# Kernel tuning notes

Hardware: AMD Instinct MI355X
Metric: run time of the kernel (lower is better)

## Reference

```python
import jax, jax.numpy as jnp
import numpy as np
import math

B, T = 8, 1024
IN_DIMS = 1024
OUT_DIMS = 1024
NUM_CODES = 1024
NUM_CODEBOOKS = 8


def setup_inputs() -> dict:
    key = jax.random.key(0)
    k1, k2, k3, k4, k5 = jax.random.split(key, 5)
    x = jax.random.normal(k1, (B, T, IN_DIMS), dtype=jnp.float32)
    target = jax.random.randint(k2, (B, T, NUM_CODEBOOKS), 0, NUM_CODES, dtype=jnp.int64)
    # params, init per reset_params()
    codebook = jax.random.normal(k3, (NUM_CODES, NUM_CODEBOOKS, OUT_DIMS), dtype=jnp.float32) / math.sqrt(OUT_DIMS * NUM_CODEBOOKS)
    proj_w = jax.random.normal(k4, (NUM_CODEBOOKS * NUM_CODES, IN_DIMS), dtype=jnp.float32) / math.sqrt(IN_DIMS)
    proj_b = jnp.zeros((NUM_CODEBOOKS * NUM_CODES,), dtype=jnp.float32)
    wproj_w = jax.random.normal(k5, (NUM_CODEBOOKS, IN_DIMS), dtype=jnp.float32) / math.sqrt(IN_DIMS)
    return {"x": x, "target": target, "codebook": codebook,
            "proj_w": proj_w, "proj_b": proj_b, "wproj_w": wproj_w}


def reference(x, target, codebook, proj_w, proj_b, wproj_w):
    # xp: (B, T, K, C)
    xp = (jnp.einsum('btd,nd->btn', x, proj_w) + proj_b).reshape(B, T, NUM_CODEBOOKS, NUM_CODES)
    # xw: (B, T, K) softmax codebook weights
    xw = jax.nn.softmax(jnp.einsum('btd,kd->btk', x, wproj_w), axis=-1)
    # gather codebook embeddings under no_grad: codebook[target, arange(K)] -> (B, T, K, D)
    cb_inds = jnp.arange(NUM_CODEBOOKS)
    codebook_embs = jax.lax.stop_gradient(codebook[target, cb_inds])
    # per-element cross entropy, reduction='none' -> (B, T, K)
    logp = jax.nn.log_softmax(xp, axis=-1)
    x_loss = -jnp.take_along_axis(logp, target[..., None], axis=-1)[..., 0]
    # softmax-weighted sum over codebooks -> (B, T, D)
    emb = jnp.einsum('btkd,btk->btd', codebook_embs, xw)
    return emb, x_loss
```

## Files before the change

kernel.cpp:

```cpp
#include <hip/hip_runtime.h>
#include <hip/hip_bf16.h>
#include <math.h>

#define MTOT   8192
#define KDIM   1024
#define NCODES 1024
#define NCB    8
#define NTOT   8192
#define ODIM   1024

typedef __attribute__((ext_vector_type(8))) short  bf16x8;
typedef __attribute__((ext_vector_type(4))) float  f32x4;

__device__ __forceinline__ ushort f2bf(float f) {
  union { float f; unsigned u; } v; v.f = f;
  unsigned u = v.u;
  unsigned r = (u + 0x7fffu + ((u >> 16) & 1u)) >> 16;
  return (ushort)r;
}

__device__ __forceinline__ void gload16(const void* g, void* l) {
  __builtin_amdgcn_global_load_lds(
      (const __attribute__((address_space(1))) void*)g,
      (__attribute__((address_space(3))) void*)l,
      16, 0, 0);
}

__global__ void cvt_bf16_kernel(const float* __restrict__ in,
                                ushort* __restrict__ out) {
  int i = blockIdx.x * blockDim.x + threadIdx.x;
  float4 v = ((const float4*)in)[i];
  ushort4 o;
  o.x = f2bf(v.x); o.y = f2bf(v.y); o.z = f2bf(v.z); o.w = f2bf(v.w);
  ((ushort4*)out)[i] = o;
}


__device__ __forceinline__ void chunk_dec(int c, int& srcA, int& srcB) {
  const int q  = c >> 6;
  const int sq = q >> 1;
  const int ct = q & 1;
  const int r4 = (c >> 2) & 15;
  const int cb = (((c & 3) ^ ((c >> 3) & 3)) << 4);
  const int rtA = (sq & 3) + ((sq >> 2) << 3);
  const int rtB = (sq & 1) + ((sq >> 1) << 2);
  srcA = ((rtA << 4) + r4) * (KDIM * 2) + ct * 64 + cb;
  srcB = ((rtB << 4) + r4) * (KDIM * 2) + ct * 64 + cb;
}

#define STAGE_A(T, H) do { \
    const int ao_ = (((T) & 15) * 128 + (H) * 131072); \
    char* ld_ = ldsA_st + ((T) & 1) * 32768 + (H) * 16384; \
    gload16(Ag + (size_t)(srcA0 + ao_), ld_); \
    gload16(Ag + (size_t)(srcA1 + ao_), ld_ + 8192); \
  } while(0)
#define STAGE_B(T, H) do { \
    const int bo_ = (((T) >> 4) * 524288 + ((T) & 15) * 128 + (H) * 65536); \
    char* ld_ = ldsB_st + ((T) & 1) * 32768 + (H) * 16384; \
    gload16(Bg + (size_t)(srcB0 + bo_), ld_); \
    gload16(Bg + (size_t)(srcB1 + bo_), ld_ + 8192); \
  } while(0)

#define LDA_Q(P, MH) do { \
    _Pragma("unroll") for (int m_ = 0; m_ < 4; ++m_) \
    _Pragma("unroll") for (int k_ = 0; k_ < 2; ++k_) \
      a[m_][k_] = *(const bf16x8*)(ldsA_rd + (P)*32768 + (MH)*16384 + m_*2048 + k_*1024); \
  } while(0)
#define LDB_Q(P, NH, B) do { \
    _Pragma("unroll") for (int n_ = 0; n_ < 2; ++n_) \
    _Pragma("unroll") for (int k_ = 0; k_ < 2; ++k_) \
      B[n_][k_] = *(const bf16x8*)(ldsB_rd + (P)*32768 + (NH)*16384 + n_*2048 + k_*1024); \
  } while(0)
#define MM_Q(MH, NH, B) do { \
    _Pragma("unroll") for (int k_ = 0; k_ < 2; ++k_) \
    _Pragma("unroll") for (int m_ = 0; m_ < 4; ++m_) \
    _Pragma("unroll") for (int n_ = 0; n_ < 2; ++n_) \
      acc[(MH)*4+m_][(NH)*2+n_] = __builtin_amdgcn_mfma_f32_16x16x32_bf16( \
          a[m_][k_], B[n_][k_], acc[(MH)*4+m_][(NH)*2+n_], 0, 0, 0); \
  } while(0)

#define PH_MID(MH, NH, B) \
    __builtin_amdgcn_s_barrier(); \
    asm volatile("s_waitcnt lgkmcnt(0)" ::: "memory"); \
    __builtin_amdgcn_sched_barrier(0); \
    __builtin_amdgcn_s_setprio(1); \
    MM_Q(MH, NH, B); \
    __builtin_amdgcn_s_setprio(0);
#define PH_END \
    __builtin_amdgcn_s_barrier(); \
    asm volatile("" ::: "memory");
#define LGKM_PACE \
    asm volatile("s_waitcnt lgkmcnt(8)" ::: "memory");

#define FLUSH(SEG) do { \
    const int colb_ = (SEG) * 256 + wc * 64; \
    float bias_n[4]; \
    _Pragma("unroll") for (int n_ = 0; n_ < 4; ++n_) \
      bias_n[n_] = bias[kcb * 1024 + colb_ + n_ * 16 + c15]; \
    _Pragma("unroll") for (int m_ = 0; m_ < 8; ++m_) { \
      _Pragma("unroll") for (int j_ = 0; j_ < 4; ++j_) { \
        const int rl_ = wr * 128 + m_ * 16 + g * 4 + j_; \
        const int tc_ = tgtcol[rl_]; \
        float s_ = 0.f; \
        _Pragma("unroll") for (int n_ = 0; n_ < 4; ++n_) { \
          const float v_ = acc[m_][n_][j_] + bias_n[n_]; \
          if (colb_ + n_ * 16 + c15 == tc_) tgtval[rl_] = v_; \
          s_ += __expf(v_); \
        } \
        _Pragma("unroll") for (int o_ = 1; o_ < 16; o_ <<= 1) \
          s_ += __shfl_xor(s_, o_); \
        if (c15 == 0) redS[wc * 256 + rl_] = s_; \
      } \
    } \
    __syncthreads(); \
    if (tid < 256) \
      S_acc += redS[tid] + redS[tid + 256] + redS[tid + 512] + redS[tid + 768]; \
    _Pragma("unroll") for (int m_ = 0; m_ < 8; ++m_) \
      _Pragma("unroll") for (int n_ = 0; n_ < 4; ++n_) \
        acc[m_][n_] = (f32x4){0.f, 0.f, 0.f, 0.f}; \
  } while(0)

__global__ __launch_bounds__(512, 2)
void ce_gemm_kernel(const ushort* __restrict__ Abf,
                    const ushort* __restrict__ Bbf,
                    const float*  __restrict__ bias,
                    const int*    __restrict__ target,
                    float* __restrict__ xloss) {
  extern __shared__ char smem[];
  float* redS   = (float*)(smem + 131072);
  int*   tgtcol = (int*)  (smem + 135168);
  float* tgtval = (float*)(smem + 136192);

  const int tid  = threadIdx.x;
  const int wid  = tid >> 6;
  const int lane = tid & 63;
  const int wr   = wid >> 2;
  const int wc   = wid & 3;
  const int g    = lane >> 4;
  const int c15  = lane & 15;
  const int bidx  = blockIdx.x;
  const int u     = bidx >> 3;
  const int mtile = (bidx & 7) * 4 + (u & 3);
  const int kcb   = u >> 2;

  const int swz = (c15 * 64 + g * 16) ^ ((c15 & 6) << 3);
  const char* ldsA_rd = smem + wr * 8192 + swz;
  const char* ldsB_rd = smem + 65536 + wc * 4096 + swz;
  char* ldsA_st = smem + wid * 1024;
  char* ldsB_st = smem + 65536 + wid * 1024;

  const char* Ag = ((const char*)Abf) + (size_t)mtile * 256 * (KDIM * 2);
  const char* Bg = ((const char*)Bbf) + (size_t)kcb * 2097152;
  int srcA0, srcB0, srcA1, srcB1;
  chunk_dec(tid,       srcA0, srcB0);
  chunk_dec(tid + 512, srcA1, srcB1);

  if (tid < 256)
    tgtcol[tid] = target[(size_t)(mtile * 256 + tid) * NCB + kcb];

  f32x4 acc[8][4];
#pragma unroll
  for (int m = 0; m < 8; ++m)
#pragma unroll
    for (int n = 0; n < 4; ++n)
      acc[m][n] = (f32x4){0.f, 0.f, 0.f, 0.f};

  float S_acc = 0.f;
  bf16x8 a[4][2], b0[2][2], b1[2][2];

  STAGE_A(0, 0); STAGE_A(0, 1); STAGE_B(0, 0); STAGE_B(0, 1);
  STAGE_A(1, 0); STAGE_B(1, 1);
  asm volatile("s_waitcnt vmcnt(4)" ::: "memory");
  __syncthreads();

#pragma unroll 1
  for (int it = 0; it < 31; ++it) {
    const int t1 = 2 * it + 1;
    LDA_Q(0, 0); LDB_Q(0, 0, b0);
    STAGE_A(t1, 1);
    LGKM_PACE
    PH_MID(0, 0, b0) PH_END
    LDB_Q(0, 1, b1);
    STAGE_B(t1, 0);
    PH_MID(0, 1, b1) PH_END
    LDA_Q(0, 1);
    STAGE_A(t1 + 1, 0);
    PH_MID(1, 1, b1) PH_END
    STAGE_B(t1 + 1, 1);
    PH_MID(1, 0, b0)
    asm volatile("s_waitcnt vmcnt(4)" ::: "memory");
    PH_END
    LDA_Q(1, 0); LDB_Q(1, 0, b0);
    STAGE_A(t1 + 1, 1);
    LGKM_PACE
    PH_MID(0, 0, b0) PH_END
    LDB_Q(1, 1, b1);
    STAGE_B(t1 + 1, 0);
    PH_MID(0, 1, b1) PH_END
    LDA_Q(1, 1);
    STAGE_A(t1 + 2, 0);
    PH_MID(1, 1, b1) PH_END
    STAGE_B(t1 + 2, 1);
    PH_MID(1, 0, b0)
    asm volatile("s_waitcnt vmcnt(4)" ::: "memory");
    PH_END

    if ((it & 7) == 7) FLUSH(it >> 3);
  }

  LDA_Q(0, 0); LDB_Q(0, 0, b0);
  STAGE_A(63, 1);
  PH_MID(0, 0, b0) PH_END
  LDB_Q(0, 1, b1);
  STAGE_B(63, 0);
  PH_MID(0, 1, b1) PH_END
  LDA_Q(0, 1);
  PH_MID(1, 1, b1) PH_END
  PH_MID(1, 0, b0)
  asm volatile("s_waitcnt vmcnt(0)" ::: "memory");
  PH_END
  LDA_Q(1, 0); LDB_Q(1, 0, b0);
  PH_MID(0, 0, b0) PH_END
  LDB_Q(1, 1, b1);
  PH_MID(0, 1, b1) PH_END
  LDA_Q(1, 1);
  PH_MID(1, 1, b1) PH_END
  PH_MID(1, 0, b0) PH_END

  FLUSH(3);
  __syncthreads();

  if (tid < 256) {
    const int row = mtile * 256 + tid;
    xloss[(size_t)row * NCB + kcb] = __logf(S_acc) - tgtval[tid];
  }
}

__global__ void emb_kernel(const float* __restrict__ x,
                           const int*   __restrict__ target,
                           const float* __restrict__ cb,
                           const float* __restrict__ wproj,
                           float* __restrict__ emb_out,
                           ushort* __restrict__ xbf) {
  const int bt   = blockIdx.x;
  const int tid  = threadIdx.x;
  const int lane = tid & 63;
  const int wid  = tid >> 6;

  const float4 xv = ((const float4*)(x + (size_t)bt * KDIM))[tid];
  ushort4 xo;
  xo.x = f2bf(xv.x); xo.y = f2bf(xv.y); xo.z = f2bf(xv.z); xo.w = f2bf(xv.w);
  ((ushort4*)(xbf + (size_t)bt * KDIM))[tid] = xo;

  float p[8];
#pragma unroll
  for (int k = 0; k < 8; ++k) {
    const float4 wv = ((const float4*)(wproj + k * KDIM))[tid];
    p[k] = xv.x * wv.x + xv.y * wv.y + xv.z * wv.z + xv.w * wv.w;
  }
#pragma unroll
  for (int k = 0; k < 8; ++k)
#pragma unroll
    for (int off = 32; off >= 1; off >>= 1)
      p[k] += __shfl_xor(p[k], off);

  __shared__ float lred[4][8];
  if (lane == 0) {
#pragma unroll
    for (int k = 0; k < 8; ++k) lred[wid][k] = p[k];
  }
  __syncthreads();

  float logit[8], mx = -1e30f;
#pragma unroll
  for (int k = 0; k < 8; ++k) {
    logit[k] = lred[0][k] + lred[1][k] + lred[2][k] + lred[3][k];
    mx = fmaxf(mx, logit[k]);
  }
  float w[8], den = 0.f;
#pragma unroll
  for (int k = 0; k < 8; ++k) { w[k] = __expf(logit[k] - mx); den += w[k]; }
  const float inv = 1.f / den;

  float4 acc = make_float4(0.f, 0.f, 0.f, 0.f);
#pragma unroll
  for (int k = 0; k < 8; ++k) {
    const int t = target[bt * NCB + k];
    const float4 cv = ((const float4*)(cb + ((size_t)t * NCB + k) * ODIM))[tid];
    const float wk = w[k] * inv;
    acc.x += wk * cv.x; acc.y += wk * cv.y; acc.z += wk * cv.z; acc.w += wk * cv.w;
  }
  ((float4*)(emb_out + (size_t)bt * ODIM))[tid] = acc;
}

extern "C" void kernel_launch(void* const* d_in, const int* in_sizes, int n_in,
                              void* d_out, int out_size, void* d_ws, size_t ws_size,
                              hipStream_t stream) {
  const float* x        = (const float*)d_in[0];
  const int*   target   = (const int*)  d_in[1];
  const float* codebook = (const float*)d_in[2];
  const float* proj_w   = (const float*)d_in[3];
  const float* proj_b   = (const float*)d_in[4];
  const float* wproj_w  = (const float*)d_in[5];

  float* out       = (float*)d_out;
  float* emb_out   = out;
  float* xloss_out = out + (size_t)MTOT * ODIM;

  char* ws = (char*)d_ws;
  ushort* xbf = (ushort*)ws;
  ushort* wbf = (ushort*)(ws + (size_t)16 * 1024 * 1024);

  hipFuncSetAttribute((const void*)ce_gemm_kernel,
                      hipFuncAttributeMaxDynamicSharedMemorySize, 137216);

  emb_kernel<<<MTOT, 256, 0, stream>>>(x, target, codebook, wproj_w, emb_out, xbf);
  cvt_bf16_kernel<<<(NTOT * KDIM / 4) / 256, 256, 0, stream>>>(proj_w, wbf);

  ce_gemm_kernel<<<256, 512, 137216, stream>>>(xbf, wbf, proj_b, target, xloss_out);
}
```

Before: 204.8 us.

## Restructure GEMM main loop into two-barrier per-tile pipeline with full register prefetch

Replaces the hand-unrolled eight-phase loop, which had a barrier before and after each quarter MFMA block, with a simpler 64-iteration loop. Each iteration loads all A/B fragments for the tile from LDS into registers up front (separate a0/a1), then runs two MFMA halves separated by a single barrier. Global-to-LDS staging of the next tiles is issued between those halves. The aim is fewer barriers and LDS waits per tile, at the cost of more VGPRs for the extra A fragment buffer and a changed staging order that must still be race-free with the double-buffered LDS. The FLUSH sync is also replaced with a raw lgkmcnt wait plus s_barrier.

```diff
diff --git a/kernel.cpp b/kernel.cpp
--- a/kernel.cpp
+++ b/kernel.cpp
@@ -61,36 +61,23 @@
     gload16(Bg + (size_t)(srcB1 + bo_), ld_ + 8192); \
   } while(0)
 
-#define LDA_Q(P, MH) do { \
+#define LDA_Q(P, MH, AR) do { \
     _Pragma("unroll") for (int m_ = 0; m_ < 4; ++m_) \
     _Pragma("unroll") for (int k_ = 0; k_ < 2; ++k_) \
-      a[m_][k_] = *(const bf16x8*)(ldsA_rd + (P)*32768 + (MH)*16384 + m_*2048 + k_*1024); \
-  } while(0)
-#define LDB_Q(P, NH, B) do { \
+      AR[m_][k_] = *(const bf16x8*)(ldsA_rd + (P)*32768 + (MH)*16384 + m_*2048 + k_*1024); \
+  } while(0)
+#define LDB_Q(P, NH, BR) do { \
     _Pragma("unroll") for (int n_ = 0; n_ < 2; ++n_) \
     _Pragma("unroll") for (int k_ = 0; k_ < 2; ++k_) \
-      B[n_][k_] = *(const bf16x8*)(ldsB_rd + (P)*32768 + (NH)*16384 + n_*2048 + k_*1024); \
-  } while(0)
-#define MM_Q(MH, NH, B) do { \
+      BR[n_][k_] = *(const bf16x8*)(ldsB_rd + (P)*32768 + (NH)*16384 + n_*2048 + k_*1024); \
+  } while(0)
+#define MM_Q(MH, NH, AR, BR) do { \
     _Pragma("unroll") for (int k_ = 0; k_ < 2; ++k_) \
     _Pragma("unroll") for (int m_ = 0; m_ < 4; ++m_) \
     _Pragma("unroll") for (int n_ = 0; n_ < 2; ++n_) \
       acc[(MH)*4+m_][(NH)*2+n_] = __builtin_amdgcn_mfma_f32_16x16x32_bf16( \
-          a[m_][k_], B[n_][k_], acc[(MH)*4+m_][(NH)*2+n_], 0, 0, 0); \
-  } while(0)
-
-#define PH_MID(MH, NH, B) \
-    __builtin_amdgcn_s_barrier(); \
-    asm volatile("s_waitcnt lgkmcnt(0)" ::: "memory"); \
-    __builtin_amdgcn_sched_barrier(0); \
-    __builtin_amdgcn_s_setprio(1); \
-    MM_Q(MH, NH, B); \
-    __builtin_amdgcn_s_setprio(0);
-#define PH_END \
-    __builtin_amdgcn_s_barrier(); \
-    asm volatile("" ::: "memory");
-#define LGKM_PACE \
-    asm volatile("s_waitcnt lgkmcnt(8)" ::: "memory");
+          AR[m_][k_], BR[n_][k_], acc[(MH)*4+m_][(NH)*2+n_], 0, 0, 0); \
+  } while(0)
 
 #define FLUSH(SEG) do { \
     const int colb_ = (SEG) * 256 + wc * 64; \
@@ -112,7 +99,8 @@
         if (c15 == 0) redS[wc * 256 + rl_] = s_; \
       } \
     } \
-    __syncthreads(); \
+    asm volatile("s_waitcnt lgkmcnt(0)" ::: "memory"); \
+    asm volatile("s_barrier" ::: "memory"); \
     if (tid < 256) \
       S_acc += redS[tid] + redS[tid + 256] + redS[tid + 512] + redS[tid + 768]; \
     _Pragma("unroll") for (int m_ = 0; m_ < 8; ++m_) \
@@ -166,70 +154,35 @@
       acc[m][n] = (f32x4){0.f, 0.f, 0.f, 0.f};
 
   float S_acc = 0.f;
-  bf16x8 a[4][2], b0[2][2], b1[2][2];
+  bf16x8 a0[4][2], a1[4][2], b0[2][2], b1[2][2];
 
   STAGE_A(0, 0); STAGE_A(0, 1); STAGE_B(0, 0); STAGE_B(0, 1);
-  STAGE_A(1, 0); STAGE_B(1, 1);
-  asm volatile("s_waitcnt vmcnt(4)" ::: "memory");
+  STAGE_A(1, 0); STAGE_B(1, 0); STAGE_B(1, 1);
+  asm volatile("s_waitcnt vmcnt(6)" ::: "memory");
   __syncthreads();
 
 #pragma unroll 1
-  for (int it = 0; it < 31; ++it) {
-    const int t1 = 2 * it + 1;
-    LDA_Q(0, 0); LDB_Q(0, 0, b0);
-    STAGE_A(t1, 1);
-    LGKM_PACE
-    PH_MID(0, 0, b0) PH_END
-    LDB_Q(0, 1, b1);
-    STAGE_B(t1, 0);
-    PH_MID(0, 1, b1) PH_END
-    LDA_Q(0, 1);
-    STAGE_A(t1 + 1, 0);
-    PH_MID(1, 1, b1) PH_END
-    STAGE_B(t1 + 1, 1);
-    PH_MID(1, 0, b0)
-    asm volatile("s_waitcnt vmcnt(4)" ::: "memory");
-    PH_END
-    LDA_Q(1, 0); LDB_Q(1, 0, b0);
-    STAGE_A(t1 + 1, 1);
-    LGKM_PACE
-    PH_MID(0, 0, b0) PH_END
-    LDB_Q(1, 1, b1);
-    STAGE_B(t1 + 1, 0);
-    PH_MID(0, 1, b1) PH_END
-    LDA_Q(1, 1);
-    STAGE_A(t1 + 2, 0);
-    PH_MID(1, 1, b1) PH_END
-    STAGE_B(t1 + 2, 1);
-    PH_MID(1, 0, b0)
-    asm volatile("s_waitcnt vmcnt(4)" ::: "memory");
-    PH_END
-
-    if ((it & 7) == 7) FLUSH(it >> 3);
-  }
-
-  LDA_Q(0, 0); LDB_Q(0, 0, b0);
-  STAGE_A(63, 1);
-  PH_MID(0, 0, b0) PH_END
-  LDB_Q(0, 1, b1);
-  STAGE_B(63, 0);
-  PH_MID(0, 1, b1) PH_END
-  LDA_Q(0, 1);
-  PH_MID(1, 1, b1) PH_END
-  PH_MID(1, 0, b0)
-  asm volatile("s_waitcnt vmcnt(0)" ::: "memory");
-  PH_END
-  LDA_Q(1, 0); LDB_Q(1, 0, b0);
-  PH_MID(0, 0, b0) PH_END
-  LDB_Q(1, 1, b1);
-  PH_MID(0, 1, b1) PH_END
-  LDA_Q(1, 1);
-  PH_MID(1, 1, b1) PH_END
-  PH_MID(1, 0, b0) PH_END
-
-  FLUSH(3);
+  for (int t = 0; t < 64; ++t) {
+    const int P = t & 1;
+    LDA_Q(P, 0, a0); LDB_Q(P, 0, b0); LDB_Q(P, 1, b1); LDA_Q(P, 1, a1);
+    if (t < 63) STAGE_A(t + 1, 1);
+    __builtin_amdgcn_s_setprio(1);
+    MM_Q(0, 0, a0, b0);
+    MM_Q(0, 1, a0, b1);
+    __builtin_amdgcn_s_setprio(0);
+    asm volatile("s_barrier" ::: "memory");
+    if (t < 62) { STAGE_A(t + 2, 0); STAGE_B(t + 2, 0); STAGE_B(t + 2, 1); }
+    __builtin_amdgcn_s_setprio(1);
+    MM_Q(1, 1, a1, b1);
+    MM_Q(1, 0, a1, b0);
+    __builtin_amdgcn_s_setprio(0);
+    if (t < 62) { asm volatile("s_waitcnt vmcnt(6)" ::: "memory"); }
+    else        { asm volatile("s_waitcnt vmcnt(0)" ::: "memory"); }
+    asm volatile("s_barrier" ::: "memory");
+    if ((t & 15) == 15) FLUSH(t >> 4);
+  }
+
   __syncthreads();
-
   if (tid < 256) {
     const int row = mtile * 256 + tid;
     xloss[(size_t)row * NCB + kcb] = __logf(S_acc) - tgtval[tid];
```

Measured after the change: 212.9 us. +3.9%, slower.

## Switch CE GEMM inner tiles from 16x16x32 to 32x32x16 bf16 MFMA

Applied to the files above, without the earlier changes.

Replaces the 16x16x32 MFMA micro-tiles with 32x32x16 MFMA instructions. This changes the accumulator layout to f32x16 per 32x32 tile, the LDS read addressing (per-k-slice swizzled offsets), and the softmax-flush row/column mapping, which now reduces over 32 lanes. The larger MFMA cuts the instruction count and LDS fragment reads per FLOP. The cost is a different register footprint and a heavier shuffle reduction in the flush. The flush's __syncthreads is also replaced by an explicit waitcnt plus s_barrier.

```diff
diff --git a/kernel.cpp b/kernel.cpp
--- a/kernel.cpp
+++ b/kernel.cpp
@@ -9,8 +9,9 @@
 #define NTOT   8192
 #define ODIM   1024
 
-typedef __attribute__((ext_vector_type(8))) short  bf16x8;
-typedef __attribute__((ext_vector_type(4))) float  f32x4;
+typedef __attribute__((ext_vector_type(8)))  short bf16x8;
+typedef __attribute__((ext_vector_type(4)))  float f32x4;
+typedef __attribute__((ext_vector_type(16))) float f32x16;
 
 __device__ __forceinline__ ushort f2bf(float f) {
   union { float f; unsigned u; } v; v.f = f;
@@ -61,30 +62,28 @@
     gload16(Bg + (size_t)(srcB1 + bo_), ld_ + 8192); \
   } while(0)
 
-#define LDA_Q(P, MH) do { \
-    _Pragma("unroll") for (int m_ = 0; m_ < 4; ++m_) \
-    _Pragma("unroll") for (int k_ = 0; k_ < 2; ++k_) \
-      a[m_][k_] = *(const bf16x8*)(ldsA_rd + (P)*32768 + (MH)*16384 + m_*2048 + k_*1024); \
-  } while(0)
-#define LDB_Q(P, NH, B) do { \
-    _Pragma("unroll") for (int n_ = 0; n_ < 2; ++n_) \
-    _Pragma("unroll") for (int k_ = 0; k_ < 2; ++k_) \
-      B[n_][k_] = *(const bf16x8*)(ldsB_rd + (P)*32768 + (NH)*16384 + n_*2048 + k_*1024); \
-  } while(0)
-#define MM_Q(MH, NH, B) do { \
-    _Pragma("unroll") for (int k_ = 0; k_ < 2; ++k_) \
-    _Pragma("unroll") for (int m_ = 0; m_ < 4; ++m_) \
-    _Pragma("unroll") for (int n_ = 0; n_ < 2; ++n_) \
-      acc[(MH)*4+m_][(NH)*2+n_] = __builtin_amdgcn_mfma_f32_16x16x32_bf16( \
-          a[m_][k_], B[n_][k_], acc[(MH)*4+m_][(NH)*2+n_], 0, 0, 0); \
-  } while(0)
-
-#define PH_MID(MH, NH, B) \
+#define LDA32(P, MH) do { \
+    _Pragma("unroll") for (int m_ = 0; m_ < 2; ++m_) \
+    _Pragma("unroll") for (int ks_ = 0; ks_ < 4; ++ks_) \
+      a[m_][ks_] = *(const bf16x8*)(ldsA_rd + (P)*32768 + (MH)*16384 + m_*4096 + iks[ks_]); \
+  } while(0)
+#define LDB32(P, N32, BR) do { \
+    _Pragma("unroll") for (int ks_ = 0; ks_ < 4; ++ks_) \
+      BR[ks_] = *(const bf16x8*)(ldsB_rd + (P)*32768 + (N32)*16384 + iks[ks_]); \
+  } while(0)
+#define MM32(MH, N32, BR) do { \
+    _Pragma("unroll") for (int ks_ = 0; ks_ < 4; ++ks_) \
+    _Pragma("unroll") for (int m_ = 0; m_ < 2; ++m_) \
+      acc[(MH)*2+m_][N32] = __builtin_amdgcn_mfma_f32_32x32x16_bf16( \
+          a[m_][ks_], BR[ks_], acc[(MH)*2+m_][N32], 0, 0, 0); \
+  } while(0)
+
+#define PH_MID(MH, N32, BR) \
     __builtin_amdgcn_s_barrier(); \
     asm volatile("s_waitcnt lgkmcnt(0)" ::: "memory"); \
     __builtin_amdgcn_sched_barrier(0); \
     __builtin_amdgcn_s_setprio(1); \
-    MM_Q(MH, NH, B); \
+    MM32(MH, N32, BR); \
     __builtin_amdgcn_s_setprio(0);
 #define PH_END \
     __builtin_amdgcn_s_barrier(); \
@@ -94,30 +93,31 @@
 
 #define FLUSH(SEG) do { \
     const int colb_ = (SEG) * 256 + wc * 64; \
-    float bias_n[4]; \
-    _Pragma("unroll") for (int n_ = 0; n_ < 4; ++n_) \
-      bias_n[n_] = bias[kcb * 1024 + colb_ + n_ * 16 + c15]; \
-    _Pragma("unroll") for (int m_ = 0; m_ < 8; ++m_) { \
-      _Pragma("unroll") for (int j_ = 0; j_ < 4; ++j_) { \
-        const int rl_ = wr * 128 + m_ * 16 + g * 4 + j_; \
+    float bias_n[2]; \
+    _Pragma("unroll") for (int n_ = 0; n_ < 2; ++n_) \
+      bias_n[n_] = bias[kcb * 1024 + colb_ + n_ * 32 + cl]; \
+    _Pragma("unroll") for (int m_ = 0; m_ < 4; ++m_) { \
+      _Pragma("unroll") for (int r_ = 0; r_ < 16; ++r_) { \
+        const int rl_ = wr * 128 + m_ * 32 + (r_ & 3) + ((r_ >> 2) << 3) + khalf * 4; \
         const int tc_ = tgtcol[rl_]; \
         float s_ = 0.f; \
-        _Pragma("unroll") for (int n_ = 0; n_ < 4; ++n_) { \
-          const float v_ = acc[m_][n_][j_] + bias_n[n_]; \
-          if (colb_ + n_ * 16 + c15 == tc_) tgtval[rl_] = v_; \
+        _Pragma("unroll") for (int n_ = 0; n_ < 2; ++n_) { \
+          const float v_ = acc[m_][n_][r_] + bias_n[n_]; \
+          if (colb_ + n_ * 32 + cl == tc_) tgtval[rl_] = v_; \
           s_ += __expf(v_); \
         } \
-        _Pragma("unroll") for (int o_ = 1; o_ < 16; o_ <<= 1) \
+        _Pragma("unroll") for (int o_ = 1; o_ < 32; o_ <<= 1) \
           s_ += __shfl_xor(s_, o_); \
-        if (c15 == 0) redS[wc * 256 + rl_] = s_; \
+        if (cl == 0) redS[wc * 256 + rl_] = s_; \
       } \
     } \
-    __syncthreads(); \
+    asm volatile("s_waitcnt lgkmcnt(0)" ::: "memory"); \
+    asm volatile("s_barrier" ::: "memory"); \
     if (tid < 256) \
       S_acc += redS[tid] + redS[tid + 256] + redS[tid + 512] + redS[tid + 768]; \
-    _Pragma("unroll") for (int m_ = 0; m_ < 8; ++m_) \
-      _Pragma("unroll") for (int n_ = 0; n_ < 4; ++n_) \
-        acc[m_][n_] = (f32x4){0.f, 0.f, 0.f, 0.f}; \
+    _Pragma("unroll") for (int m_ = 0; m_ < 4; ++m_) \
+      _Pragma("unroll") for (int n_ = 0; n_ < 2; ++n_) \
+        acc[m_][n_] = (f32x16)(0.f); \
   } while(0)
 
 __global__ __launch_bounds__(512, 2)
@@ -131,21 +131,28 @@
   int*   tgtcol = (int*)  (smem + 135168);
   float* tgtval = (float*)(smem + 136192);
 
-  const int tid  = threadIdx.x;
-  const int wid  = tid >> 6;
-  const int lane = tid & 63;
-  const int wr   = wid >> 2;
-  const int wc   = wid & 3;
-  const int g    = lane >> 4;
-  const int c15  = lane & 15;
+  const int tid   = threadIdx.x;
+  const int wid   = tid >> 6;
+  const int lane  = tid & 63;
+  const int wr    = wid >> 2;
+  const int wc    = wid & 3;
+  const int c15   = lane & 15;
+  const int rhalf = (lane >> 4) & 1;
+  const int khalf = lane >> 5;
+  const int cl    = lane & 31;
   const int bidx  = blockIdx.x;
   const int u     = bidx >> 3;
   const int mtile = (bidx & 7) * 4 + (u & 3);
   const int kcb   = u >> 2;
 
-  const int swz = (c15 * 64 + g * 16) ^ ((c15 & 6) << 3);
-  const char* ldsA_rd = smem + wr * 8192 + swz;
-  const char* ldsB_rd = smem + 65536 + wc * 4096 + swz;
+  const int xo = (c15 & 6) << 3;
+  int iks[4];
+#pragma unroll
+  for (int ks = 0; ks < 4; ++ks)
+    iks[ks] = (ks >> 1) * 1024 + ((c15 * 64 + (ks & 1) * 32 + khalf * 16) ^ xo);
+
+  const char* ldsA_rd = smem + wr * 8192 + rhalf * 2048;
+  const char* ldsB_rd = smem + 65536 + wc * 4096 + rhalf * 2048;
   char* ldsA_st = smem + wid * 1024;
   char* ldsB_st = smem + 65536 + wid * 1024;
 
@@ -158,15 +165,15 @@
   if (tid < 256)
     tgtcol[tid] = target[(size_t)(mtile * 256 + tid) * NCB + kcb];
 
-  f32x4 acc[8][4];
-#pragma unroll
-  for (int m = 0; m < 8; ++m)
-#pragma unroll
-    for (int n = 0; n < 4; ++n)
-      acc[m][n] = (f32x4){0.f, 0.f, 0.f, 0.f};
+  f32x16 acc[4][2];
+#pragma unroll
+  for (int m = 0; m < 4; ++m)
+#pragma unroll
+    for (int n = 0; n < 2; ++n)
+      acc[m][n] = (f32x16)(0.f);
 
   float S_acc = 0.f;
-  bf16x8 a[4][2], b0[2][2], b1[2][2];
+  bf16x8 a[2][4], b0[4], b1[4];
 
   STAGE_A(0, 0); STAGE_A(0, 1); STAGE_B(0, 0); STAGE_B(0, 1);
   STAGE_A(1, 0); STAGE_B(1, 1);
@@ -176,28 +183,28 @@
 #pragma unroll 1
   for (int it = 0; it < 31; ++it) {
     const int t1 = 2 * it + 1;
-    LDA_Q(0, 0); LDB_Q(0, 0, b0);
+    LDA32(0, 0); LDB32(0, 0, b0);
     STAGE_A(t1, 1);
     LGKM_PACE
     PH_MID(0, 0, b0) PH_END
-    LDB_Q(0, 1, b1);
+    LDB32(0, 1, b1);
     STAGE_B(t1, 0);
     PH_MID(0, 1, b1) PH_END
-    LDA_Q(0, 1);
+    LDA32(0, 1);
     STAGE_A(t1 + 1, 0);
     PH_MID(1, 1, b1) PH_END
     STAGE_B(t1 + 1, 1);
     PH_MID(1, 0, b0)
     asm volatile("s_waitcnt vmcnt(4)" ::: "memory");
     PH_END
-    LDA_Q(1, 0); LDB_Q(1, 0, b0);
+    LDA32(1, 0); LDB32(1, 0, b0);
     STAGE_A(t1 + 1, 1);
     LGKM_PACE
     PH_MID(0, 0, b0) PH_END
-    LDB_Q(1, 1, b1);
+    LDB32(1, 1, b1);
     STAGE_B(t1 + 1, 0);
     PH_MID(0, 1, b1) PH_END
-    LDA_Q(1, 1);
+    LDA32(1, 1);
     STAGE_A(t1 + 2, 0);
     PH_MID(1, 1, b1) PH_END
     STAGE_B(t1 + 2, 1);
@@ -208,22 +215,22 @@
     if ((it & 7) == 7) FLUSH(it >> 3);
   }
 
-  LDA_Q(0, 0); LDB_Q(0, 0, b0);
+  LDA32(0, 0); LDB32(0, 0, b0);
   STAGE_A(63, 1);
   PH_MID(0, 0, b0) PH_END
-  LDB_Q(0, 1, b1);
+  LDB32(0, 1, b1);
   STAGE_B(63, 0);
   PH_MID(0, 1, b1) PH_END
-  LDA_Q(0, 1);
+  LDA32(0, 1);
   PH_MID(1, 1, b1) PH_END
   PH_MID(1, 0, b0)
   asm volatile("s_waitcnt vmcnt(0)" ::: "memory");
   PH_END
-  LDA_Q(1, 0); LDB_Q(1, 0, b0);
+  LDA32(1, 0); LDB32(1, 0, b0);
   PH_MID(0, 0, b0) PH_END
-  LDB_Q(1, 1, b1);
+  LDB32(1, 1, b1);
   PH_MID(0, 1, b1) PH_END
-  LDA_Q(1, 1);
+  LDA32(1, 1);
   PH_MID(1, 1, b1) PH_END
   PH_MID(1, 0, b0) PH_END
 
```

Measured after the change: 284.2 us. 1.39x slower.
